# Kernel tuning notes

Measured on AMD Instinct MI355X. Metric: run time of the kernel, lower is better.

Reference implementation:

```python
import jax, jax.numpy as jnp
import numpy as np


def setup_inputs() -> dict:
    key = jax.random.key(0)
    k1, k2, k3 = jax.random.split(key, 3)
    B, IN, H, OUT = 2048, 4096, 4096, 1024
    x = jax.random.normal(k1, (B, IN), dtype=jnp.float32)
    fc1_weight = jax.random.randint(k2, (H, IN), 0, 2).astype(jnp.int32)
    fc2_weight = jax.random.randint(k3, (OUT, H), 0, 2).astype(jnp.int32)
    return {"x": x, "fc1_weight": fc1_weight, "fc2_weight": fc2_weight, "threshold": 2048}


def _binary_popcount_matmul(a, w):
    # a: (B, K) in {0,1}, w: (N, K) in {0,1}
    # matches = sum_k 1 - (a XOR w) = a@w.T + (1-a)@(1-w).T  (identical math,
    # avoids materializing the (B, N, K) XNOR tensor the naive code builds)
    return jnp.einsum('bk,nk->bn', a, w) + jnp.einsum('bk,nk->bn', 1 - a, 1 - w)


def reference(x, fc1_weight, fc2_weight, threshold):
    xb = (x.reshape(x.shape[0], -1) >= 0).astype(jnp.int32)   # binarize input
    pc1 = _binary_popcount_matmul(xb, fc1_weight)              # (B, H) popcounts
    act1 = (pc1 >= threshold).astype(jnp.int32)                # threshold activation
    pc2 = _binary_popcount_matmul(act1, fc2_weight)            # (B, OUT) popcounts
    return pc2
```

## Files before the change

kernel.cpp:

```cpp
#include <hip/hip_runtime.h>
#include <stdint.h>

typedef int v4i  __attribute__((ext_vector_type(4)));
typedef int v16i __attribute__((ext_vector_type(16)));

__device__ __forceinline__ void gload_lds16(const void* g, void* l) {
    __builtin_amdgcn_global_load_lds(
        (const __attribute__((address_space(1))) void*)g,
        (__attribute__((address_space(3))) void*)l, 16, 0, 0);
}

template<typename T, bool ISFLOAT>
__global__ __launch_bounds__(512)
void pack_frag(const T* __restrict__ in, int8_t* __restrict__ F, int K) {
    __shared__ int8_t lbuf[32 * 1040];
    const int t  = threadIdx.x;
    const int db = blockIdx.y;
    const int c0 = blockIdx.x << 10;

    #pragma unroll
    for (int p = 0; p < 16; ++p) {
        int idx = p * 512 + t;
        int row = idx >> 8, c4 = idx & 255;
        uint32_t b;
        if constexpr (ISFLOAT) {
            const float4 v = *(const float4*)(in + (size_t)(db * 32 + row) * K + c0 + c4 * 4);
            b =  (v.x >= 0.0f ? 0x01u : 0xFFu)
              | ((v.y >= 0.0f ? 0x01u : 0xFFu) << 8)
              | ((v.z >= 0.0f ? 0x01u : 0xFFu) << 16)
              | ((v.w >= 0.0f ? 0x01u : 0xFFu) << 24);
        } else {
            const int4 v = *(const int4*)(in + (size_t)(db * 32 + row) * K + c0 + c4 * 4);
            b =  (v.x ? 0x01u : 0xFFu)
              | ((v.y ? 0x01u : 0xFFu) << 8)
              | ((v.z ? 0x01u : 0xFFu) << 16)
              | ((v.w ? 0x01u : 0xFFu) << 24);
        }
        *(uint32_t*)(lbuf + row * 1040 + c4 * 4) = b;
    }
    __syncthreads();

    const int s  = t >> 4;
    const int l0 = (t & 15) * 4;
    const int KC = K >> 5;
    int8_t* dst = F + ((size_t)db * KC + blockIdx.x * 32 + s) * 1024;
    #pragma unroll
    for (int li = 0; li < 4; ++li) {
        int l = l0 + li;
        uint4 v = *(const uint4*)(lbuf + (l & 31) * 1040 + s * 32 + (l >> 5) * 16);
        *(uint4*)(dst + l * 16) = v;
    }
}

__global__ __launch_bounds__(512, 2)
void bnn_l1_8w(const int8_t* __restrict__ Af,
               const int8_t* __restrict__ Bf,
               const int* __restrict__ thr_ptr,
               int8_t* __restrict__ actf)
{
    constexpr int KC  = 128;
    constexpr int NKT = 64;
    constexpr uint32_t BUFSZ = 24576;

    __shared__ int8_t lds[3 * 24576];

    const int tid  = threadIdx.x;
    const int lane = tid & 63;
    const int wv   = tid >> 6;
    const int wr   = wv >> 2, wc = wv & 3;

    const int g   = blockIdx.x;
    const int idx = g >> 3;
    const int bn  = (g & 7) * 2 + (idx >> 4);
    const int bm  = idx & 15;

    const int8_t* gsrc[3];
    uint32_t loff[3];
    #pragma unroll
    for (int c = 0; c < 3; ++c) {
        int s = c * 512 + tid;
        if (s < 512) {
            int R = s >> 7, kk = (s >> 6) & 1, ln = s & 63;
            gsrc[c] = Af + ((size_t)(bm * 4 + R) * KC + kk) * 1024 + ln * 16;
            loff[c] = (uint32_t)s * 16;
        } else {
            int s2 = s - 512;
            int Cb = s2 >> 7, kk = (s2 >> 6) & 1, ln = s2 & 63;
            gsrc[c] = Bf + ((size_t)(bn * 8 + Cb) * KC + kk) * 1024 + ln * 16;
            loff[c] = 8192u + (uint32_t)s2 * 16;
        }
    }

    auto issue = [&](int c, uint32_t bufo) {
        gload_lds16(gsrc[c], lds + bufo + loff[c]);
        gsrc[c] += 2048;
    };

    v16i acc[2][2];
    #pragma unroll
    for (int i = 0; i < 2; ++i)
        #pragma unroll
        for (int j = 0; j < 2; ++j) acc[i][j] = {};

    issue(0, 0); issue(1, 0); issue(2, 0);
    issue(0, BUFSZ); issue(1, BUFSZ); issue(2, BUFSZ);

    uint32_t bo = 0;
    #pragma unroll 1
    for (int kt = 0; kt < NKT; ++kt) {
        if (kt + 1 < NKT) asm volatile("s_waitcnt vmcnt(3)" ::: "memory");
        else              asm volatile("s_waitcnt vmcnt(0)" ::: "memory");
        __builtin_amdgcn_sched_barrier(0);
        __builtin_amdgcn_s_barrier();
        __builtin_amdgcn_sched_barrier(0);

        const uint32_t sbo = (bo >= BUFSZ) ? (bo - BUFSZ) : (2 * BUFSZ);
        const int8_t* Ab = lds + bo + wr * 4096 + lane * 16;
        const int8_t* Bb = lds + bo + 8192 + wc * 4096 + lane * 16;

        {
            v4i af0 = *(const v4i*)(Ab + 0);
            v4i af1 = *(const v4i*)(Ab + 2048);
            v4i bf0 = *(const v4i*)(Bb + 0);
            v4i bf1 = *(const v4i*)(Bb + 2048);
            if (kt + 2 < NKT) { issue(0, sbo); issue(1, sbo); }
            __builtin_amdgcn_s_barrier();
            asm volatile("s_waitcnt lgkmcnt(0)" ::: "memory");
            __builtin_amdgcn_sched_barrier(0);
            __builtin_amdgcn_s_setprio(1);
            acc[0][0] = __builtin_amdgcn_mfma_i32_32x32x32_i8(af0, bf0, acc[0][0], 0, 0, 0);
            acc[0][1] = __builtin_amdgcn_mfma_i32_32x32x32_i8(af0, bf1, acc[0][1], 0, 0, 0);
            acc[1][0] = __builtin_amdgcn_mfma_i32_32x32x32_i8(af1, bf0, acc[1][0], 0, 0, 0);
            acc[1][1] = __builtin_amdgcn_mfma_i32_32x32x32_i8(af1, bf1, acc[1][1], 0, 0, 0);
            __builtin_amdgcn_s_setprio(0);
            __builtin_amdgcn_sched_barrier(0);
            __builtin_amdgcn_s_barrier();
        }
        {
            v4i af0 = *(const v4i*)(Ab + 1024);
            v4i af1 = *(const v4i*)(Ab + 3072);
            v4i bf0 = *(const v4i*)(Bb + 1024);
            v4i bf1 = *(const v4i*)(Bb + 3072);
            if (kt + 2 < NKT) issue(2, sbo);
            __builtin_amdgcn_s_barrier();
            asm volatile("s_waitcnt lgkmcnt(0)" ::: "memory");
            __builtin_amdgcn_sched_barrier(0);
            __builtin_amdgcn_s_setprio(1);
            acc[0][0] = __builtin_amdgcn_mfma_i32_32x32x32_i8(af0, bf0, acc[0][0], 0, 0, 0);
            acc[0][1] = __builtin_amdgcn_mfma_i32_32x32x32_i8(af0, bf1, acc[0][1], 0, 0, 0);
            acc[1][0] = __builtin_amdgcn_mfma_i32_32x32x32_i8(af1, bf0, acc[1][0], 0, 0, 0);
            acc[1][1] = __builtin_amdgcn_mfma_i32_32x32x32_i8(af1, bf1, acc[1][1], 0, 0, 0);
            __builtin_amdgcn_s_setprio(0);
            __builtin_amdgcn_sched_barrier(0);
        }
        bo = (bo == 2 * BUFSZ) ? 0u : bo + BUFSZ;
    }

    __syncthreads();
    const int thr = *thr_ptr;
    int8_t* bits = lds;
    #pragma unroll
    for (int i = 0; i < 2; ++i)
        #pragma unroll
        for (int j = 0; j < 2; ++j) {
            int dimb = wr * 64 + i * 32 + 4 * (lane >> 5);
            int gcl  = wc * 64 + j * 32 + (lane & 31);
            #pragma unroll
            for (int reg = 0; reg < 16; ++reg) {
                int dl = dimb + (reg & 3) + 8 * (reg >> 2);
                int match = (4096 + acc[i][j][reg]) >> 1;
                bits[dl * 272 + gcl] = (match >= thr) ? (int8_t)1 : (int8_t)-1;
            }
        }
    __syncthreads();
    const int s    = tid >> 4;
    const int dblk = s >> 3, kcl = s & 7;
    const int l0   = (tid & 15) * 4;
    int8_t* dst = actf + ((size_t)(bm * 4 + dblk) * KC + bn * 8 + kcl) * 1024;
    #pragma unroll
    for (int li = 0; li < 4; ++li) {
        int l = l0 + li;
        uint4 v = *(const uint4*)(bits + (dblk * 32 + (l & 31)) * 272
                                       + kcl * 32 + (l >> 5) * 16);
        *(uint4*)(dst + l * 16) = v;
    }
}

template<int WN>
__global__ __launch_bounds__(256, 1)
void bnn_mfma2(const int8_t* __restrict__ Af,
               const int8_t* __restrict__ Bf,
               int* __restrict__ out, int Nout)
{
    constexpr int KC     = 128;
    constexpr int NKT    = 64;
    constexpr int NBB    = 2 * WN;
    constexpr int ASLOTS = 512;
    constexpr int BSLOTS = 128 * NBB;
    constexpr int SLOTS  = ASLOTS + BSLOTS;
    constexpr int NLD    = SLOTS / 256;
    constexpr uint32_t BUFSZ = (uint32_t)SLOTS * 16;

    __shared__ int8_t lds[3][SLOTS * 16];

    const int tid  = threadIdx.x;
    const int lane = tid & 63;
    const int wv   = tid >> 6;
    const int wr   = wv >> 1, wc = wv & 1;

    const int g   = blockIdx.x;
    const int idx = g >> 3;
    const int bn  = (g & 7) * 2 + (idx >> 4);
    const int bm  = idx & 15;

    const int8_t* gsrc[NLD];
    uint32_t ldoff[NLD];
    #pragma unroll
    for (int i = 0; i < NLD; ++i) {
        int sbase = wv * 64 + 256 * i;
        ldoff[i] = (uint32_t)sbase * 16;
        const int8_t* base;
        if (sbase < ASLOTS) {
            int R = sbase >> 7, C = (sbase >> 6) & 1;
            base = Af + ((size_t)(bm * 4 + R) * KC + C) * 1024;
        } else {
            int s = sbase - ASLOTS;
            int R = s >> 7, C = (s >> 6) & 1;
            base = Bf + ((size_t)(bn * NBB + R) * KC + C) * 1024;
        }
        gsrc[i] = base + lane * 16;
    }

    auto stage = [&](int buf) {
        #pragma unroll
        for (int i = 0; i < NLD; ++i) {
            gload_lds16(gsrc[i], (int8_t*)lds + (uint32_t)buf * BUFSZ + ldoff[i]);
            gsrc[i] += 2048;
        }
    };

    v16i acc[2][WN];
    #pragma unroll
    for (int i = 0; i < 2; ++i)
        #pragma unroll
        for (int j = 0; j < WN; ++j) acc[i][j] = {};

    stage(0);
    stage(1);

    int cur = 0, nxt = 2;
    #pragma unroll 1
    for (int kt = 0; kt < NKT; ++kt) {
        if (kt < NKT - 1) asm volatile("s_waitcnt vmcnt(3)" ::: "memory");
        else              asm volatile("s_waitcnt vmcnt(0)" ::: "memory");
        __builtin_amdgcn_sched_barrier(0);
        __builtin_amdgcn_s_barrier();
        __builtin_amdgcn_sched_barrier(0);

        if (kt < NKT - 2) {
            stage(nxt);
            nxt = (nxt == 2) ? 0 : nxt + 1;
        }

        const int8_t* Al = lds[cur];
        const int8_t* Bl = lds[cur] + ASLOTS * 16;
        #pragma unroll
        for (int kc = 0; kc < 2; ++kc) {
            v4i af[2], bf[WN];
            #pragma unroll
            for (int i = 0; i < 2; ++i)
                af[i] = *(const v4i*)(Al + (((wr * 2 + i) * 2 + kc) * 64 + lane) * 16);
            #pragma unroll
            for (int j = 0; j < WN; ++j)
                bf[j] = *(const v4i*)(Bl + (((wc * WN + j) * 2 + kc) * 64 + lane) * 16);
            #pragma unroll
            for (int i = 0; i < 2; ++i)
                #pragma unroll
                for (int j = 0; j < WN; ++j)
                    acc[i][j] = __builtin_amdgcn_mfma_i32_32x32x32_i8(af[i], bf[j], acc[i][j], 0, 0, 0);
        }
        cur = (cur == 2) ? 0 : cur + 1;
    }

    #pragma unroll
    for (int i = 0; i < 2; ++i)
        #pragma unroll
        for (int j = 0; j < WN; ++j) {
            int gc = bn * (64 * WN) + wc * (32 * WN) + j * 32 + (lane & 31);
            #pragma unroll
            for (int reg = 0; reg < 16; ++reg) {
                int gr = bm * 128 + wr * 64 + i * 32
                       + (reg & 3) + 8 * (reg >> 2) + 4 * (lane >> 5);
                out[(size_t)gr * Nout + gc] = (4096 + acc[i][j][reg]) >> 1;
            }
        }
}

extern "C" void kernel_launch(void* const* d_in, const int* in_sizes, int n_in,
                              void* d_out, int out_size, void* d_ws, size_t ws_size,
                              hipStream_t stream) {
    const float* x   = (const float*)d_in[0];
    const int*   w1  = (const int*)d_in[1];
    const int*   w2  = (const int*)d_in[2];
    const int*   thr = (const int*)d_in[3];
    int* out = (int*)d_out;

    const int B = 2048, IN = 4096, H = 4096, OUT = 1024;
    uint8_t* ws = (uint8_t*)d_ws;

    int8_t* Af  = (int8_t*)(ws);
    int8_t* W1f = (int8_t*)(ws + ((size_t)8  << 20));
    int8_t* W2f = (int8_t*)(ws + ((size_t)24 << 20));
    int8_t* Act = (int8_t*)(ws + ((size_t)28 << 20));

    pack_frag<float, true ><<<dim3(IN / 1024, B   / 32), 512, 0, stream>>>(x,  Af,  IN);
    pack_frag<int,   false><<<dim3(IN / 1024, H   / 32), 512, 0, stream>>>(w1, W1f, IN);
    pack_frag<int,   false><<<dim3(H  / 1024, OUT / 32), 512, 0, stream>>>(w2, W2f, H);

    bnn_l1_8w<<<256, 512, 0, stream>>>(Af, W1f, thr, Act);
    bnn_mfma2<1><<<256, 256, 0, stream>>>(Act, W2f, out, OUT);
}
```

Measured before the change: 92.15 us.

## Load layer-1 A fragments straight to registers and halve block tile

```diff
diff --git a/kernel.cpp b/kernel.cpp
--- a/kernel.cpp
+++ b/kernel.cpp
@@ -52,49 +52,40 @@
     }
 }
 
-__global__ __launch_bounds__(512, 2)
-void bnn_l1_8w(const int8_t* __restrict__ Af,
-               const int8_t* __restrict__ Bf,
-               const int* __restrict__ thr_ptr,
-               int8_t* __restrict__ actf)
+__global__ __launch_bounds__(256, 2)
+void bnn_l1_areg(const int8_t* __restrict__ Af,
+                 const int8_t* __restrict__ Bf,
+                 const int* __restrict__ thr_ptr,
+                 int8_t* __restrict__ actf)
 {
     constexpr int KC  = 128;
     constexpr int NKT = 64;
-    constexpr uint32_t BUFSZ = 24576;
-
-    __shared__ int8_t lds[3 * 24576];
+    constexpr uint32_t BUFSZ = 8192;
+
+    __shared__ int8_t lds[3 * 8192];
 
     const int tid  = threadIdx.x;
     const int lane = tid & 63;
     const int wv   = tid >> 6;
-    const int wr   = wv >> 2, wc = wv & 3;
+    const int wr   = wv >> 1, wc = wv & 1;
 
     const int g   = blockIdx.x;
     const int idx = g >> 3;
-    const int bn  = (g & 7) * 2 + (idx >> 4);
+    const int bn  = (g & 7) * 4 + (idx >> 4);
     const int bm  = idx & 15;
 
-    const int8_t* gsrc[3];
-    uint32_t loff[3];
-    #pragma unroll
-    for (int c = 0; c < 3; ++c) {
-        int s = c * 512 + tid;
-        if (s < 512) {
-            int R = s >> 7, kk = (s >> 6) & 1, ln = s & 63;
-            gsrc[c] = Af + ((size_t)(bm * 4 + R) * KC + kk) * 1024 + ln * 16;
-            loff[c] = (uint32_t)s * 16;
-        } else {
-            int s2 = s - 512;
-            int Cb = s2 >> 7, kk = (s2 >> 6) & 1, ln = s2 & 63;
-            gsrc[c] = Bf + ((size_t)(bn * 8 + Cb) * KC + kk) * 1024 + ln * 16;
-            loff[c] = 8192u + (uint32_t)s2 * 16;
-        }
-    }
-
-    auto issue = [&](int c, uint32_t bufo) {
-        gload_lds16(gsrc[c], lds + bufo + loff[c]);
-        gsrc[c] += 2048;
-    };
+    const int8_t* gB0; const int8_t* gB1;
+    uint32_t lo0, lo1;
+    {
+        int s0 = tid;
+        gB0 = Bf + ((size_t)(bn * 4 + (s0 >> 7)) * KC + ((s0 >> 6) & 1)) * 1024 + (s0 & 63) * 16;
+        lo0 = (uint32_t)s0 * 16;
+        int s1 = tid + 256;
+        gB1 = Bf + ((size_t)(bn * 4 + (s1 >> 7)) * KC + ((s1 >> 6) & 1)) * 1024 + (s1 & 63) * 16;
+        lo1 = (uint32_t)s1 * 16;
+    }
+
+    const int8_t* gA = Af + ((size_t)(bm * 4 + wr * 2) * KC) * 1024 + lane * 16;
 
     v16i acc[2][2];
     #pragma unroll
@@ -102,58 +93,67 @@
         #pragma unroll
         for (int j = 0; j < 2; ++j) acc[i][j] = {};
 
-    issue(0, 0); issue(1, 0); issue(2, 0);
-    issue(0, BUFSZ); issue(1, BUFSZ); issue(2, BUFSZ);
+    v4i aA0 = *(const v4i*)(gA);
+    v4i aA1 = *(const v4i*)(gA + 1024);
+    v4i aA2 = *(const v4i*)(gA + 131072);
+    v4i aA3 = *(const v4i*)(gA + 132096);
+    gload_lds16(gB0, lds + lo0);         gB0 += 2048;
+    gload_lds16(gB1, lds + lo1);         gB1 += 2048;
+    gload_lds16(gB0, lds + BUFSZ + lo0); gB0 += 2048;
+    gload_lds16(gB1, lds + BUFSZ + lo1); gB1 += 2048;
+    v4i aB0{}, aB1{}, aB2{}, aB3{};
 
     uint32_t bo = 0;
-    #pragma unroll 1
-    for (int kt = 0; kt < NKT; ++kt) {
-        if (kt + 1 < NKT) asm volatile("s_waitcnt vmcnt(3)" ::: "memory");
+
+    auto kt_body = [&](int kt, v4i& AR0, v4i& AR1, v4i& AR2, v4i& AR3,
+                               v4i& AW0, v4i& AW1, v4i& AW2, v4i& AW3) {
+        if (kt + 1 < NKT) asm volatile("s_waitcnt vmcnt(2)" ::: "memory");
         else              asm volatile("s_waitcnt vmcnt(0)" ::: "memory");
         __builtin_amdgcn_sched_barrier(0);
         __builtin_amdgcn_s_barrier();
         __builtin_amdgcn_sched_barrier(0);
 
-        const uint32_t sbo = (bo >= BUFSZ) ? (bo - BUFSZ) : (2 * BUFSZ);
-        const int8_t* Ab = lds + bo + wr * 4096 + lane * 16;
-        const int8_t* Bb = lds + bo + 8192 + wc * 4096 + lane * 16;
-
-        {
-            v4i af0 = *(const v4i*)(Ab + 0);
-            v4i af1 = *(const v4i*)(Ab + 2048);
-            v4i bf0 = *(const v4i*)(Bb + 0);
-            v4i bf1 = *(const v4i*)(Bb + 2048);
-            if (kt + 2 < NKT) { issue(0, sbo); issue(1, sbo); }
-            __builtin_amdgcn_s_barrier();
-            asm volatile("s_waitcnt lgkmcnt(0)" ::: "memory");
+        const uint32_t sbo = (bo >= BUFSZ) ? (bo - BUFSZ) : (2u * BUFSZ);
+        const int8_t* Bb = lds + bo + wc * 4096 + lane * 16;
+
+        v4i bf00 = *(const v4i*)(Bb + 0);
+        v4i bf10 = *(const v4i*)(Bb + 2048);
+        __builtin_amdgcn_s_setprio(1);
+        acc[0][0] = __builtin_amdgcn_mfma_i32_32x32x32_i8(AR0, bf00, acc[0][0], 0, 0, 0);
+        acc[0][1] = __builtin_amdgcn_mfma_i32_32x32x32_i8(AR0, bf10, acc[0][1], 0, 0, 0);
+        acc[1][0] = __builtin_amdgcn_mfma_i32_32x32x32_i8(AR2, bf00, acc[1][0], 0, 0, 0);
+        acc[1][1] = __builtin_amdgcn_mfma_i32_32x32x32_i8(AR2, bf10, acc[1][1], 0, 0, 0);
+        __builtin_amdgcn_s_setprio(0);
+
+        if (kt + 1 < NKT) {
+            const int8_t* ga = gA + (kt + 1) * 2048;
+            AW0 = *(const v4i*)(ga);
+            AW1 = *(const v4i*)(ga + 1024);
+            AW2 = *(const v4i*)(ga + 131072);
+            AW3 = *(const v4i*)(ga + 132096);
             __builtin_amdgcn_sched_barrier(0);
-            __builtin_amdgcn_s_setprio(1);
-            acc[0][0] = __builtin_amdgcn_mfma_i32_32x32x32_i8(af0, bf0, acc[0][0], 0, 0, 0);
-            acc[0][1] = __builtin_amdgcn_mfma_i32_32x32x32_i8(af0, bf1, acc[0][1], 0, 0, 0);
-            acc[1][0] = __builtin_amdgcn_mfma_i32_32x32x32_i8(af1, bf0, acc[1][0], 0, 0, 0);
-            acc[1][1] = __builtin_amdgcn_mfma_i32_32x32x32_i8(af1, bf1, acc[1][1], 0, 0, 0);
-            __builtin_amdgcn_s_setprio(0);
-            __builtin_amdgcn_sched_barrier(0);
-            __builtin_amdgcn_s_barrier();
-        }
-        {
-            v4i af0 = *(const v4i*)(Ab + 1024);
-            v4i af1 = *(const v4i*)(Ab + 3072);
-            v4i bf0 = *(const v4i*)(Bb + 1024);
-            v4i bf1 = *(const v4i*)(Bb + 3072);
-            if (kt + 2 < NKT) issue(2, sbo);
-            __builtin_amdgcn_s_barrier();
-            asm volatile("s_waitcnt lgkmcnt(0)" ::: "memory");
-            __builtin_amdgcn_sched_barrier(0);
-            __builtin_amdgcn_s_setprio(1);
-            acc[0][0] = __builtin_amdgcn_mfma_i32_32x32x32_i8(af0, bf0, acc[0][0], 0, 0, 0);
-            acc[0][1] = __builtin_amdgcn_mfma_i32_32x32x32_i8(af0, bf1, acc[0][1], 0, 0, 0);
-            acc[1][0] = __builtin_amdgcn_mfma_i32_32x32x32_i8(af1, bf0, acc[1][0], 0, 0, 0);
-            acc[1][1] = __builtin_amdgcn_mfma_i32_32x32x32_i8(af1, bf1, acc[1][1], 0, 0, 0);
-            __builtin_amdgcn_s_setprio(0);
-            __builtin_amdgcn_sched_barrier(0);
-        }
-        bo = (bo == 2 * BUFSZ) ? 0u : bo + BUFSZ;
+        }
+        if (kt + 2 < NKT) {
+            gload_lds16(gB0, lds + sbo + lo0); gB0 += 2048;
+            gload_lds16(gB1, lds + sbo + lo1); gB1 += 2048;
+        }
+
+        v4i bf01 = *(const v4i*)(Bb + 1024);
+        v4i bf11 = *(const v4i*)(Bb + 3072);
+        __builtin_amdgcn_s_setprio(1);
+        acc[0][0] = __builtin_amdgcn_mfma_i32_32x32x32_i8(AR1, bf01, acc[0][0], 0, 0, 0);
+        acc[0][1] = __builtin_amdgcn_mfma_i32_32x32x32_i8(AR1, bf11, acc[0][1], 0, 0, 0);
+        acc[1][0] = __builtin_amdgcn_mfma_i32_32x32x32_i8(AR3, bf01, acc[1][0], 0, 0, 0);
+        acc[1][1] = __builtin_amdgcn_mfma_i32_32x32x32_i8(AR3, bf11, acc[1][1], 0, 0, 0);
+        __builtin_amdgcn_s_setprio(0);
+
+        bo = (bo == 2u * BUFSZ) ? 0u : bo + BUFSZ;
+    };
+
+    #pragma unroll 1
+    for (int kt = 0; kt < NKT; kt += 2) {
+        kt_body(kt,     aA0, aA1, aA2, aA3, aB0, aB1, aB2, aB3);
+        kt_body(kt + 1, aB0, aB1, aB2, aB3, aA0, aA1, aA2, aA3);
     }
 
     __syncthreads();
@@ -169,18 +169,18 @@
             for (int reg = 0; reg < 16; ++reg) {
                 int dl = dimb + (reg & 3) + 8 * (reg >> 2);
                 int match = (4096 + acc[i][j][reg]) >> 1;
-                bits[dl * 272 + gcl] = (match >= thr) ? (int8_t)1 : (int8_t)-1;
+                bits[dl * 144 + gcl] = (match >= thr) ? (int8_t)1 : (int8_t)-1;
             }
         }
     __syncthreads();
     const int s    = tid >> 4;
-    const int dblk = s >> 3, kcl = s & 7;
+    const int dblk = s >> 2, kcl = s & 3;
     const int l0   = (tid & 15) * 4;
-    int8_t* dst = actf + ((size_t)(bm * 4 + dblk) * KC + bn * 8 + kcl) * 1024;
+    int8_t* dst = actf + ((size_t)(bm * 4 + dblk) * KC + bn * 4 + kcl) * 1024;
     #pragma unroll
     for (int li = 0; li < 4; ++li) {
         int l = l0 + li;
-        uint4 v = *(const uint4*)(bits + (dblk * 32 + (l & 31)) * 272
+        uint4 v = *(const uint4*)(bits + (dblk * 32 + (l & 31)) * 144
                                        + kcl * 32 + (l >> 5) * 16);
         *(uint4*)(dst + l * 16) = v;
     }
@@ -317,6 +317,6 @@
     pack_frag<int,   false><<<dim3(IN / 1024, H   / 32), 512, 0, stream>>>(w1, W1f, IN);
     pack_frag<int,   false><<<dim3(H  / 1024, OUT / 32), 512, 0, stream>>>(w2, W2f, H);
 
-    bnn_l1_8w<<<256, 512, 0, stream>>>(Af, W1f, thr, Act);
+    bnn_l1_areg<<<512, 256, 0, stream>>>(Af, W1f, thr, Act);
     bnn_mfma2<1><<<256, 256, 0, stream>>>(Act, W2f, out, OUT);
 }
```

Measured after the change: 92.07 us. Within noise of the previous version (-0.1%).

## Deepen layer-1 GEMM pipeline to quad-buffered LDS with one barrier per step

Applied to the files above, without the earlier changes.

```diff
diff --git a/kernel.cpp b/kernel.cpp
--- a/kernel.cpp
+++ b/kernel.cpp
@@ -52,17 +52,17 @@
     }
 }
 
-__global__ __launch_bounds__(512, 2)
-void bnn_l1_8w(const int8_t* __restrict__ Af,
-               const int8_t* __restrict__ Bf,
-               const int* __restrict__ thr_ptr,
-               int8_t* __restrict__ actf)
+__global__ __launch_bounds__(512, 1)
+void bnn_l1_opt(const int8_t* __restrict__ Af,
+                const int8_t* __restrict__ Bf,
+                const int* __restrict__ thr_ptr,
+                int8_t* __restrict__ actf)
 {
     constexpr int KC  = 128;
     constexpr int NKT = 64;
     constexpr uint32_t BUFSZ = 24576;
 
-    __shared__ int8_t lds[3 * 24576];
+    __shared__ int8_t lds[4 * 24576];
 
     const int tid  = threadIdx.x;
     const int lane = tid & 63;
@@ -91,9 +91,10 @@
         }
     }
 
-    auto issue = [&](int c, uint32_t bufo) {
-        gload_lds16(gsrc[c], lds + bufo + loff[c]);
-        gsrc[c] += 2048;
+    auto issue3 = [&](uint32_t bufo) {
+        gload_lds16(gsrc[0], lds + bufo + loff[0]); gsrc[0] += 2048;
+        gload_lds16(gsrc[1], lds + bufo + loff[1]); gsrc[1] += 2048;
+        gload_lds16(gsrc[2], lds + bufo + loff[2]); gsrc[2] += 2048;
     };
 
     v16i acc[2][2];
@@ -102,59 +103,54 @@
         #pragma unroll
         for (int j = 0; j < 2; ++j) acc[i][j] = {};
 
-    issue(0, 0); issue(1, 0); issue(2, 0);
-    issue(0, BUFSZ); issue(1, BUFSZ); issue(2, BUFSZ);
-
-    uint32_t bo = 0;
+    issue3(0);
+    issue3(BUFSZ);
+    issue3(2 * BUFSZ);
+
+#define KT_BODY(KT, P)                                                         \
+    {                                                                          \
+        const int kt_ = (KT);                                                  \
+        if (kt_ < NKT - 2)       asm volatile("s_waitcnt vmcnt(6)" ::: "memory"); \
+        else if (kt_ == NKT - 2) asm volatile("s_waitcnt vmcnt(3)" ::: "memory"); \
+        else                     asm volatile("s_waitcnt vmcnt(0)" ::: "memory"); \
+        __builtin_amdgcn_sched_barrier(0);                                     \
+        __builtin_amdgcn_s_barrier();                                          \
+        __builtin_amdgcn_sched_barrier(0);                                     \
+        const int8_t* Ab = lds + (P) * 24576 + wr * 4096 + lane * 16;          \
+        const int8_t* Bb = lds + (P) * 24576 + 8192 + wc * 4096 + lane * 16;   \
+        v4i a00 = *(const v4i*)(Ab + 0);                                       \
+        v4i a01 = *(const v4i*)(Ab + 1024);                                    \
+        v4i a10 = *(const v4i*)(Ab + 2048);                                    \
+        v4i a11 = *(const v4i*)(Ab + 3072);                                    \
+        v4i b00 = *(const v4i*)(Bb + 0);                                       \
+        v4i b01 = *(const v4i*)(Bb + 1024);                                    \
+        v4i b10 = *(const v4i*)(Bb + 2048);                                    \
+        v4i b11 = *(const v4i*)(Bb + 3072);                                    \
+        if (kt_ + 3 < NKT) issue3(((P) + 3) % 4 * 24576u);                     \
+        __builtin_amdgcn_sched_barrier(0);                                     \
+        asm volatile("s_waitcnt lgkmcnt(0)" ::: "memory");                     \
+        __builtin_amdgcn_sched_barrier(0);                                     \
+        __builtin_amdgcn_s_setprio(1);                                         \
+        acc[0][0] = __builtin_amdgcn_mfma_i32_32x32x32_i8(a00, b00, acc[0][0], 0, 0, 0); \
+        acc[0][1] = __builtin_amdgcn_mfma_i32_32x32x32_i8(a00, b10, acc[0][1], 0, 0, 0); \
+        acc[1][0] = __builtin_amdgcn_mfma_i32_32x32x32_i8(a10, b00, acc[1][0], 0, 0, 0); \
+        acc[1][1] = __builtin_amdgcn_mfma_i32_32x32x32_i8(a10, b10, acc[1][1], 0, 0, 0); \
+        acc[0][0] = __builtin_amdgcn_mfma_i32_32x32x32_i8(a01, b01, acc[0][0], 0, 0, 0); \
+        acc[0][1] = __builtin_amdgcn_mfma_i32_32x32x32_i8(a01, b11, acc[0][1], 0, 0, 0); \
+        acc[1][0] = __builtin_amdgcn_mfma_i32_32x32x32_i8(a11, b01, acc[1][0], 0, 0, 0); \
+        acc[1][1] = __builtin_amdgcn_mfma_i32_32x32x32_i8(a11, b11, acc[1][1], 0, 0, 0); \
+        __builtin_amdgcn_s_setprio(0);                                         \
+        __builtin_amdgcn_sched_barrier(0);                                     \
+    }
+
     #pragma unroll 1
-    for (int kt = 0; kt < NKT; ++kt) {
-        if (kt + 1 < NKT) asm volatile("s_waitcnt vmcnt(3)" ::: "memory");
-        else              asm volatile("s_waitcnt vmcnt(0)" ::: "memory");
-        __builtin_amdgcn_sched_barrier(0);
-        __builtin_amdgcn_s_barrier();
-        __builtin_amdgcn_sched_barrier(0);
-
-        const uint32_t sbo = (bo >= BUFSZ) ? (bo - BUFSZ) : (2 * BUFSZ);
-        const int8_t* Ab = lds + bo + wr * 4096 + lane * 16;
-        const int8_t* Bb = lds + bo + 8192 + wc * 4096 + lane * 16;
-
-        {
-            v4i af0 = *(const v4i*)(Ab + 0);
-            v4i af1 = *(const v4i*)(Ab + 2048);
-            v4i bf0 = *(const v4i*)(Bb + 0);
-            v4i bf1 = *(const v4i*)(Bb + 2048);
-            if (kt + 2 < NKT) { issue(0, sbo); issue(1, sbo); }
-            __builtin_amdgcn_s_barrier();
-            asm volatile("s_waitcnt lgkmcnt(0)" ::: "memory");
-            __builtin_amdgcn_sched_barrier(0);
-            __builtin_amdgcn_s_setprio(1);
-            acc[0][0] = __builtin_amdgcn_mfma_i32_32x32x32_i8(af0, bf0, acc[0][0], 0, 0, 0);
-            acc[0][1] = __builtin_amdgcn_mfma_i32_32x32x32_i8(af0, bf1, acc[0][1], 0, 0, 0);
-            acc[1][0] = __builtin_amdgcn_mfma_i32_32x32x32_i8(af1, bf0, acc[1][0], 0, 0, 0);
-            acc[1][1] = __builtin_amdgcn_mfma_i32_32x32x32_i8(af1, bf1, acc[1][1], 0, 0, 0);
-            __builtin_amdgcn_s_setprio(0);
-            __builtin_amdgcn_sched_barrier(0);
-            __builtin_amdgcn_s_barrier();
-        }
-        {
-            v4i af0 = *(const v4i*)(Ab + 1024);
-            v4i af1 = *(const v4i*)(Ab + 3072);
-            v4i bf0 = *(const v4i*)(Bb + 1024);
-            v4i bf1 = *(const v4i*)(Bb + 3072);
-            if (kt + 2 < NKT) issue(2, sbo);
-            __builtin_amdgcn_s_barrier();
-            asm volatile("s_waitcnt lgkmcnt(0)" ::: "memory");
-            __builtin_amdgcn_sched_barrier(0);
-            __builtin_amdgcn_s_setprio(1);
-            acc[0][0] = __builtin_amdgcn_mfma_i32_32x32x32_i8(af0, bf0, acc[0][0], 0, 0, 0);
-            acc[0][1] = __builtin_amdgcn_mfma_i32_32x32x32_i8(af0, bf1, acc[0][1], 0, 0, 0);
-            acc[1][0] = __builtin_amdgcn_mfma_i32_32x32x32_i8(af1, bf0, acc[1][0], 0, 0, 0);
-            acc[1][1] = __builtin_amdgcn_mfma_i32_32x32x32_i8(af1, bf1, acc[1][1], 0, 0, 0);
-            __builtin_amdgcn_s_setprio(0);
-            __builtin_amdgcn_sched_barrier(0);
-        }
-        bo = (bo == 2 * BUFSZ) ? 0u : bo + BUFSZ;
-    }
+    for (int kt0 = 0; kt0 < NKT; kt0 += 4) {
+        KT_BODY(kt0 + 0, 0)
+        KT_BODY(kt0 + 1, 1)
+        KT_BODY(kt0 + 2, 2)
+        KT_BODY(kt0 + 3, 3)
+    }
+#undef KT_BODY
 
     __syncthreads();
     const int thr = *thr_ptr;
@@ -317,6 +313,6 @@
     pack_frag<int,   false><<<dim3(IN / 1024, H   / 32), 512, 0, stream>>>(w1, W1f, IN);
     pack_frag<int,   false><<<dim3(H  / 1024, OUT / 32), 512, 0, stream>>>(w2, W2f, H);
 
-    bnn_l1_8w<<<256, 512, 0, stream>>>(Af, W1f, thr, Act);
+    bnn_l1_opt<<<256, 512, 0, stream>>>(Af, W1f, thr, Act);
     bnn_mfma2<1><<<256, 256, 0, stream>>>(Act, W2f, out, OUT);
 }
```

New measurement: 88.15 us. -4.3%, faster.
